# Kernel tuning notes

Measured on AMD Instinct MI355X. Metric: run time of the kernel, lower is better.

The kernel has to match this reference:

```python
import jax, jax.numpy as jnp
import numpy as np

B, S, D, H = 4, 2048, 1024, 16
DH = D // H
MAX_SEQ = 2048
OUT = 1024


def setup_inputs() -> dict:
    key = jax.random.key(0)
    ks = jax.random.split(key, 10)
    inp = {
        "x": jax.random.normal(ks[0], (B, S, D), dtype=jnp.float32),
        "src_key_padding_mask": jnp.ones((B, S), dtype=jnp.float32),  # 1 = valid token
        "pos_emb": jax.random.normal(ks[1], (1, MAX_SEQ, D), dtype=jnp.float32),
        "ln_gamma": jnp.ones((D,), dtype=jnp.float32),
        "ln_beta": jnp.zeros((D,), dtype=jnp.float32),
        "in_proj_weight": jax.random.normal(ks[2], (3 * D, D), dtype=jnp.float32) * (1.0 / np.sqrt(D)),
        "in_proj_bias": jnp.zeros((3 * D,), dtype=jnp.float32),
        "out_proj_weight": jax.random.normal(ks[3], (D, D), dtype=jnp.float32) * (1.0 / np.sqrt(D)),
        "out_proj_bias": jnp.zeros((D,), dtype=jnp.float32),
        "to_out_weight": jax.random.normal(ks[4], (OUT, D), dtype=jnp.float32) * (1.0 / np.sqrt(D)),
        "to_out_bias": jnp.zeros((OUT,), dtype=jnp.float32),
    }
    return inp


def _layernorm(x, gamma, beta, eps=1e-5):
    mu = jnp.mean(x, axis=-1, keepdims=True)
    var = jnp.mean(jnp.square(x - mu), axis=-1, keepdims=True)
    return (x - mu) * jax.lax.rsqrt(var + eps) * gamma + beta


def reference(x, src_key_padding_mask, pos_emb, ln_gamma, ln_beta,
              in_proj_weight, in_proj_bias, out_proj_weight, out_proj_bias,
              to_out_weight, to_out_bias):
    seq = x.shape[1]
    xn = _layernorm(x, ln_gamma, ln_beta)
    xp = xn + pos_emb[:, :seq, :]  # [B,S,D]

    # PyTorch quirk: 1.0 - mask.long() is a FLOAT tensor -> treated as ADDITIVE mask.
    add_mask = (1.0 - src_key_padding_mask)[:, None, None, :]  # [B,1,1,S]

    qkv = xp @ in_proj_weight.T + in_proj_bias  # [B,S,3D]
    q, k, v = jnp.split(qkv, 3, axis=-1)
    # [B,H,S,DH]
    q = q.reshape(B, seq, H, DH).transpose(0, 2, 1, 3)
    k = k.reshape(B, seq, H, DH).transpose(0, 2, 1, 3)
    v = v.reshape(B, seq, H, DH).transpose(0, 2, 1, 3)

    scores = jnp.einsum("bhqd,bhkd->bhqk", q, k) / jnp.sqrt(jnp.float32(DH))
    scores = scores + add_mask
    attn = jax.nn.softmax(scores, axis=-1)
    o = jnp.einsum("bhqk,bhkd->bhqd", attn, v)  # [B,H,S,DH]
    o = o.transpose(0, 2, 1, 3).reshape(B, seq, D)
    attn_out = o @ out_proj_weight.T + out_proj_bias

    return (xp + attn_out) @ to_out_weight.T + to_out_bias
```

## Files before the change

kernel.cpp:

```cpp
#include <hip/hip_runtime.h>
#include <stdint.h>
#include <stddef.h>

typedef unsigned short u16;
typedef __bf16 bf16x8 __attribute__((ext_vector_type(8)));
typedef float floatx4 __attribute__((ext_vector_type(4)));

#define B_  4
#define S_  2048
#define D_  1024
#define H_  16
#define DH_ 64

__device__ __forceinline__ float b2f(u16 u) {
  union { unsigned u; float f; } c; c.u = ((unsigned)u) << 16; return c.f;
}
__device__ __forceinline__ u16 f2b(float f) {
  union { float f; unsigned u; } c; c.f = f;
  unsigned u = c.u;
  u += 0x7fffu + ((u >> 16) & 1u);
  return (u16)(u >> 16);
}

__device__ __forceinline__ void gld_lds16(const u16* g, u16* l) {
  __builtin_amdgcn_global_load_lds(
      (const __attribute__((address_space(1))) unsigned int*)g,
      (__attribute__((address_space(3))) unsigned int*)l, 16, 0, 0);
}

__device__ __forceinline__ unsigned cvtpk(float lo, float hi) {
  unsigned r;
  asm("v_cvt_pk_bf16_f32 %0, %1, %2" : "=v"(r) : "v"(lo), "v"(hi));
  return r;
}

#define PL32(a, b) asm("v_permlane32_swap_b32 %0, %1" : "+v"(a), "+v"(b))
#define PL16(a, b) asm("v_permlane16_swap_b32 %0, %1" : "+v"(a), "+v"(b))

union B8 { unsigned u[4]; bf16x8 v; };

__global__ __launch_bounds__(256) void cvt_f32_bf16(
    const float* __restrict__ src, u16* __restrict__ dst, int n)
{
  int i = (blockIdx.x * 256 + threadIdx.x) * 4;
  if (i >= n) return;
  float4 v = *(const float4*)(src + i);
  u16 o[4] __attribute__((aligned(8)));
  o[0] = f2b(v.x); o[1] = f2b(v.y); o[2] = f2b(v.z); o[3] = f2b(v.w);
  *(uint2*)(dst + i) = *(uint2*)o;
}

__global__ __launch_bounds__(256) void ln_pos_kernel(
    const float* __restrict__ x, const float* __restrict__ pos,
    const float* __restrict__ gamma, const float* __restrict__ beta,
    u16* __restrict__ xp)
{
  const int row = blockIdx.x;
  const int s = row & (S_ - 1);
  const int t = threadIdx.x;
  const int lane = t & 63, w = t >> 6;

  float4 xv = *(const float4*)(x + (size_t)row * D_ + t * 4);
  float f[4] = {xv.x, xv.y, xv.z, xv.w};
  float sum = f[0] + f[1] + f[2] + f[3];
  float sq  = f[0]*f[0] + f[1]*f[1] + f[2]*f[2] + f[3]*f[3];
#pragma unroll
  for (int m = 1; m < 64; m <<= 1) {
    sum += __shfl_xor(sum, m);
    sq  += __shfl_xor(sq, m);
  }
  __shared__ float red[8];
  if (lane == 0) { red[w] = sum; red[4 + w] = sq; }
  __syncthreads();
  sum = red[0] + red[1] + red[2] + red[3];
  sq  = red[4] + red[5] + red[6] + red[7];
  const float mu = sum * (1.f / D_);
  const float rstd = rsqrtf(fmaxf(sq * (1.f / D_) - mu * mu, 0.f) + 1e-5f);

  float4 gv = *(const float4*)(gamma + t * 4);
  float4 bv = *(const float4*)(beta + t * 4);
  float4 pv = *(const float4*)(pos + (size_t)s * D_ + t * 4);
  float g[4] = {gv.x, gv.y, gv.z, gv.w};
  float bb[4] = {bv.x, bv.y, bv.z, bv.w};
  float pp[4] = {pv.x, pv.y, pv.z, pv.w};
  u16 ov[4] __attribute__((aligned(8)));
#pragma unroll
  for (int i = 0; i < 4; ++i)
    ov[i] = f2b((f[i] - mu) * rstd * g[i] + bb[i] + pp[i]);
  *(uint2*)(xp + (size_t)row * D_ + t * 4) = *(uint2*)ov;
}

template<int HAS_BIAS, int HAS_RES, int OUT_F32>
__global__ __launch_bounds__(256) void gemm_bt(
    const u16* A, const u16* __restrict__ Bm,
    const float* __restrict__ bias, const u16* res,
    void* Cv, int M, int N, int K, int lda, int ldc)
{
  __shared__ u16 As[2][128 * 32];
  __shared__ u16 Bs[2][128 * 32];
  const int tid = threadIdx.x;
  const int lane = tid & 63, w = tid >> 6;
  const int quad = lane >> 4, l4 = lane & 15;
  const int wm = (w >> 1) * 64, wn = (w & 1) * 64;
  const int m0 = blockIdx.y * 128, n0 = blockIdx.x * 128;

  const u16* Ag = A + (size_t)m0 * lda;
  const u16* Bg = Bm + (size_t)n0 * K;

  const int s0 = tid, s1 = tid + 256;
  const int r0 = s0 >> 2, c0 = ((s0 & 3) - (r0 >> 1)) & 3;
  const int r1 = s1 >> 2, c1 = ((s1 & 3) - (r1 >> 1)) & 3;
  const int pA = (quad + (l4 >> 1)) & 3;

  floatx4 acc[4][4] = {};

  const int nk = K >> 5;
  gld_lds16(Ag + (size_t)r0 * lda + c0 * 8, &As[0][s0 * 8]);
  gld_lds16(Ag + (size_t)r1 * lda + c1 * 8, &As[0][s1 * 8]);
  gld_lds16(Bg + (size_t)r0 * K + c0 * 8, &Bs[0][s0 * 8]);
  gld_lds16(Bg + (size_t)r1 * K + c1 * 8, &Bs[0][s1 * 8]);
  __syncthreads();

  for (int kk = 0; kk < nk; ++kk) {
    const int cur = kk & 1;
    if (kk + 1 < nk) {
      const int k0 = (kk + 1) << 5;
      gld_lds16(Ag + (size_t)r0 * lda + k0 + c0 * 8, &As[cur ^ 1][s0 * 8]);
      gld_lds16(Ag + (size_t)r1 * lda + k0 + c1 * 8, &As[cur ^ 1][s1 * 8]);
      gld_lds16(Bg + (size_t)r0 * K + k0 + c0 * 8, &Bs[cur ^ 1][s0 * 8]);
      gld_lds16(Bg + (size_t)r1 * K + k0 + c1 * 8, &Bs[cur ^ 1][s1 * 8]);
    }
    bf16x8 af[4], bfr[4];
#pragma unroll
    for (int i = 0; i < 4; ++i)
      af[i] = *(const bf16x8*)&As[cur][(wm + i * 16 + l4) * 32 + pA * 8];
#pragma unroll
    for (int j = 0; j < 4; ++j)
      bfr[j] = *(const bf16x8*)&Bs[cur][(wn + j * 16 + l4) * 32 + pA * 8];
#pragma unroll
    for (int i = 0; i < 4; ++i)
#pragma unroll
      for (int j = 0; j < 4; ++j)
        acc[i][j] = __builtin_amdgcn_mfma_f32_16x16x32_bf16(af[i], bfr[j], acc[i][j], 0, 0, 0);
    __syncthreads();
  }

#pragma unroll
  for (int i = 0; i < 4; ++i) {
#pragma unroll
    for (int j = 0; j < 4; ++j) {
      const int col = n0 + wn + j * 16 + l4;
      float bvv = 0.f;
      if (HAS_BIAS) bvv = bias[col];
#pragma unroll
      for (int r = 0; r < 4; ++r) {
        const int row = m0 + wm + i * 16 + quad * 4 + r;
        float v = acc[i][j][r] + bvv;
        if (HAS_RES) v += b2f(res[(size_t)row * ldc + col]);
        v = fminf(fmaxf(v, -60000.f), 60000.f);
        if (OUT_F32) ((float*)Cv)[(size_t)row * ldc + col] = v;
        else         ((u16*)Cv)[(size_t)row * ldc + col] = f2b(v);
      }
    }
  }
}

__global__ __launch_bounds__(256, 3) void attn_kernel(
    u16* qkv, const float* __restrict__ mask)
{
  __shared__ u16 Ks[2][64 * 64];
  __shared__ u16 Vt[2][64 * 72];

  const int tid = threadIdx.x;
  const int lane = tid & 63, w = tid >> 6;
  const int quad = lane >> 4, l4 = lane & 15;
  const int qb = blockIdx.x;
  const int bh = blockIdx.y;
  const int b = bh >> 4, h = bh & 15;
  const int q0 = qb * 128;

  const size_t rstr = 3 * D_;
  u16* qbase = qkv + (size_t)b * S_ * rstr + h * DH_;

  bf16x8 qfrag[2][2];
#pragma unroll
  for (int qi = 0; qi < 2; ++qi) {
    const u16* qp = qbase + (size_t)(q0 + w * 32 + qi * 16 + l4) * rstr + quad * 8;
    qfrag[qi][0] = *(const bf16x8*)(qp);
    qfrag[qi][1] = *(const bf16x8*)(qp + 32);
  }

  const u16* kbase0 = qkv + (size_t)b * S_ * rstr + D_ + h * DH_;
  const u16* vbase0 = kbase0 + D_;
  const int vs = tid & 63, vd0 = (tid >> 6) * 16;

  floatx4 acc_o[2][4] = {};
  float l_run[2] = {0.f, 0.f};
  u16 vreg[16] __attribute__((aligned(16)));

  {
#pragma unroll
    for (int t = 0; t < 2; ++t) {
      int sidx = tid + t * 256;
      int rr = sidx >> 3, ch = ((sidx & 7) - rr) & 7;
      gld_lds16(kbase0 + (size_t)rr * rstr + ch * 8, &Ks[0][sidx * 8]);
    }
    const u16* vp = vbase0 + (size_t)vs * rstr + vd0;
    *(uint4*)(vreg)     = *(const uint4*)(vp);
    *(uint4*)(vreg + 8) = *(const uint4*)(vp + 8);
  }
  __syncthreads();
#pragma unroll
  for (int d = 0; d < 16; ++d) Vt[0][(vd0 + d) * 72 + vs] = vreg[d];
  __syncthreads();

  int cur = 0;
  for (int j = 0; j < 32; ++j) {
    if (j < 31) {
      const u16* vp = vbase0 + ((size_t)(j + 1) * 64 + vs) * rstr + vd0;
      *(uint4*)(vreg)     = *(const uint4*)(vp);
      *(uint4*)(vreg + 8) = *(const uint4*)(vp + 8);
      const u16* kb = kbase0 + (size_t)(j + 1) * 64 * rstr;
#pragma unroll
      for (int t = 0; t < 2; ++t) {
        int sidx = tid + t * 256;
        int rr = sidx >> 3, ch = ((sidx & 7) - rr) & 7;
        gld_lds16(kb + (size_t)rr * rstr + ch * 8, &Ks[cur ^ 1][sidx * 8]);
      }
    }

    floatx4 accs[2][4] = {};
#pragma unroll
    for (int kc = 0; kc < 2; ++kc)
#pragma unroll
      for (int tj = 0; tj < 4; ++tj) {
        const int rk = tj * 16 + l4;
        bf16x8 kf = *(const bf16x8*)&Ks[cur][rk * 64 + (((kc * 4 + quad) + rk) & 7) * 8];
        accs[0][tj] = __builtin_amdgcn_mfma_f32_16x16x32_bf16(kf, qfrag[0][kc], accs[0][tj], 0, 0, 0);
        accs[1][tj] = __builtin_amdgcn_mfma_f32_16x16x32_bf16(kf, qfrag[1][kc], accs[1][tj], 0, 0, 0);
      }

    const float* mrow = mask + (size_t)b * S_ + j * 64 + quad * 4;
    float4 mv[4];
#pragma unroll
    for (int tj = 0; tj < 4; ++tj) mv[tj] = *(const float4*)(mrow + tj * 16);
    unsigned pk[2][4][2];
#pragma unroll
    for (int qi = 0; qi < 2; ++qi) {
      float rsum = 0.f;
#pragma unroll
      for (int tj = 0; tj < 4; ++tj) {
        float p0 = __expf(fminf(fmaf(accs[qi][tj][0], 0.125f, 1.0f - mv[tj].x), 30.f));
        float p1 = __expf(fminf(fmaf(accs[qi][tj][1], 0.125f, 1.0f - mv[tj].y), 30.f));
        float p2 = __expf(fminf(fmaf(accs[qi][tj][2], 0.125f, 1.0f - mv[tj].z), 30.f));
        float p3 = __expf(fminf(fmaf(accs[qi][tj][3], 0.125f, 1.0f - mv[tj].w), 30.f));
        rsum += (p0 + p1) + (p2 + p3);
        pk[qi][tj][0] = cvtpk(p0, p1);
        pk[qi][tj][1] = cvtpk(p2, p3);
      }
      rsum += __shfl_xor(rsum, 16);
      rsum += __shfl_xor(rsum, 32);
      l_run[qi] += rsum;
    }

#pragma unroll
    for (int kc = 0; kc < 2; ++kc) {
      bf16x8 bfr[4];
#pragma unroll
      for (int tn = 0; tn < 4; ++tn)
        bfr[tn] = *(const bf16x8*)&Vt[cur][(tn * 16 + l4) * 72 + kc * 32 + quad * 8];
#pragma unroll
      for (int qi = 0; qi < 2; ++qi) {
        unsigned x0 = pk[qi][2 * kc][0], x1 = pk[qi][2 * kc + 1][0];
        unsigned y0 = pk[qi][2 * kc][1], y1 = pk[qi][2 * kc + 1][1];
        PL32(x0, x1); PL32(y0, y1);
        PL16(x0, x1); PL16(y0, y1);
        B8 pa; pa.u[0] = x0; pa.u[1] = y0; pa.u[2] = x1; pa.u[3] = y1;
        __builtin_amdgcn_s_setprio(1);
#pragma unroll
        for (int tn = 0; tn < 4; ++tn)
          acc_o[qi][tn] = __builtin_amdgcn_mfma_f32_16x16x32_bf16(pa.v, bfr[tn], acc_o[qi][tn], 0, 0, 0);
        __builtin_amdgcn_s_setprio(0);
      }
    }

    if (j < 31) {
#pragma unroll
      for (int d = 0; d < 16; ++d) Vt[cur ^ 1][(vd0 + d) * 72 + vs] = vreg[d];
    }

    __syncthreads();
    cur ^= 1;
  }

#pragma unroll
  for (int qi = 0; qi < 2; ++qi) {
    float inv[4];
#pragma unroll
    for (int r = 0; r < 4; ++r) inv[r] = 1.0f / __shfl(l_run[qi], quad * 4 + r);
#pragma unroll
    for (int tn = 0; tn < 4; ++tn) {
#pragma unroll
      for (int r = 0; r < 4; ++r) {
        const int row = q0 + w * 32 + qi * 16 + quad * 4 + r;
        const int col = h * DH_ + tn * 16 + l4;
        qkv[((size_t)b * S_ + row) * rstr + col] = f2b(acc_o[qi][tn][r] * inv[r]);
      }
    }
  }
}

extern "C" void kernel_launch(void* const* d_in, const int* in_sizes, int n_in,
                              void* d_out, int out_size, void* d_ws, size_t ws_size,
                              hipStream_t stream) {
  const float* x    = (const float*)d_in[0];
  const float* mask = (const float*)d_in[1];
  const float* pos  = (const float*)d_in[2];
  const float* gam  = (const float*)d_in[3];
  const float* bet  = (const float*)d_in[4];
  const float* wqkv = (const float*)d_in[5];
  const float* bqkv = (const float*)d_in[6];
  const float* wo   = (const float*)d_in[7];
  const float* bo   = (const float*)d_in[8];
  const float* wt   = (const float*)d_in[9];
  const float* bt   = (const float*)d_in[10];
  float* out = (float*)d_out;

  char* ws = (char*)d_ws;
  u16* qkvb = (u16*)(ws);
  u16* xp   = (u16*)(ws + (size_t)50331648);

  u16* wqkv_b = (u16*)d_out;
  u16* wo_b   = (u16*)((char*)d_out + (size_t)6291456);
  u16* wt_b   = qkvb;

  const int nqkv = 3 * D_ * D_;
  const int nd   = D_ * D_;

  cvt_f32_bf16<<<nqkv / 1024, 256, 0, stream>>>(wqkv, wqkv_b, nqkv);
  cvt_f32_bf16<<<nd   / 1024, 256, 0, stream>>>(wo,   wo_b,   nd);
  ln_pos_kernel<<<B_ * S_, 256, 0, stream>>>(x, pos, gam, bet, xp);
  gemm_bt<1, 0, 0><<<dim3(3 * D_ / 128, B_ * S_ / 128), 256, 0, stream>>>(
      xp, wqkv_b, bqkv, nullptr, qkvb, B_ * S_, 3 * D_, D_, D_, 3 * D_);
  attn_kernel<<<dim3(S_ / 128, B_ * H_), 256, 0, stream>>>(qkvb, mask);
  gemm_bt<1, 1, 0><<<dim3(D_ / 128, B_ * S_ / 128), 256, 0, stream>>>(
      qkvb, wo_b, bo, xp, xp, B_ * S_, D_, D_, 3 * D_, D_);
  cvt_f32_bf16<<<nd / 1024, 256, 0, stream>>>(wt, wt_b, nd);
  gemm_bt<1, 0, 1><<<dim3(D_ / 128, B_ * S_ / 128), 256, 0, stream>>>(
      xp, wt_b, bt, nullptr, out, B_ * S_, D_, D_, D_, D_);
}
```

Measured before the change: 396.9 us.

## Use exp2 softmax, MFMA row sums, and swizzled GEMM block order

The attention softmax now folds log2(e) into the score scale and the mask term and calls the raw v_exp_f32 instruction, replacing __expf. The row sums are no longer built with adds and cross-lane shuffles; an extra MFMA against a vector of bf16 ones accumulates them on the matrix unit. This also means the denominator is summed from the bf16-rounded probabilities, the same values used in P·V. Separately, the GEMM remaps block indices in groups of 8 to change L2 locality, adding integer divide and modulo work per block.

```diff
diff --git a/kernel.cpp b/kernel.cpp
--- a/kernel.cpp
+++ b/kernel.cpp
@@ -32,6 +32,10 @@
   unsigned r;
   asm("v_cvt_pk_bf16_f32 %0, %1, %2" : "=v"(r) : "v"(lo), "v"(hi));
   return r;
+}
+
+__device__ __forceinline__ float fexp2(float x) {
+  float r; asm("v_exp_f32 %0, %1" : "=v"(r) : "v"(x)); return r;
 }
 
 #define PL32(a, b) asm("v_permlane32_swap_b32 %0, %1" : "+v"(a), "+v"(b))
@@ -102,7 +106,11 @@
   const int lane = tid & 63, w = tid >> 6;
   const int quad = lane >> 4, l4 = lane & 15;
   const int wm = (w >> 1) * 64, wn = (w & 1) * 64;
-  const int m0 = blockIdx.y * 128, n0 = blockIdx.x * 128;
+
+  const int gx = gridDim.x;
+  int lin = blockIdx.y * gx + blockIdx.x;
+  lin = (lin & 7) * ((gx * gridDim.y) >> 3) + (lin >> 3);
+  const int m0 = (lin / gx) * 128, n0 = (lin % gx) * 128;
 
   const u16* Ag = A + (size_t)m0 * lda;
   const u16* Bg = Bm + (size_t)n0 * K;
@@ -194,8 +202,11 @@
   const u16* vbase0 = kbase0 + D_;
   const int vs = tid & 63, vd0 = (tid >> 6) * 16;
 
+  B8 ones;
+  ones.u[0] = ones.u[1] = ones.u[2] = ones.u[3] = 0x3f803f80u;
+
   floatx4 acc_o[2][4] = {};
-  float l_run[2] = {0.f, 0.f};
+  floatx4 acc_l[2] = {};
   u16 vreg[16] __attribute__((aligned(16)));
 
   {
@@ -241,26 +252,27 @@
       }
 
     const float* mrow = mask + (size_t)b * S_ + j * 64 + quad * 4;
-    float4 mv[4];
-#pragma unroll
-    for (int tj = 0; tj < 4; ++tj) mv[tj] = *(const float4*)(mrow + tj * 16);
+    float mterm[4][4];
+#pragma unroll
+    for (int tj = 0; tj < 4; ++tj) {
+      float4 mv = *(const float4*)(mrow + tj * 16);
+      mterm[tj][0] = fmaf(mv.x, -1.44269504f, 1.44269504f);
+      mterm[tj][1] = fmaf(mv.y, -1.44269504f, 1.44269504f);
+      mterm[tj][2] = fmaf(mv.z, -1.44269504f, 1.44269504f);
+      mterm[tj][3] = fmaf(mv.w, -1.44269504f, 1.44269504f);
+    }
     unsigned pk[2][4][2];
 #pragma unroll
     for (int qi = 0; qi < 2; ++qi) {
-      float rsum = 0.f;
 #pragma unroll
       for (int tj = 0; tj < 4; ++tj) {
-        float p0 = __expf(fminf(fmaf(accs[qi][tj][0], 0.125f, 1.0f - mv[tj].x), 30.f));
-        float p1 = __expf(fminf(fmaf(accs[qi][tj][1], 0.125f, 1.0f - mv[tj].y), 30.f));
-        float p2 = __expf(fminf(fmaf(accs[qi][tj][2], 0.125f, 1.0f - mv[tj].z), 30.f));
-        float p3 = __expf(fminf(fmaf(accs[qi][tj][3], 0.125f, 1.0f - mv[tj].w), 30.f));
-        rsum += (p0 + p1) + (p2 + p3);
+        float p0 = fexp2(fminf(fmaf(accs[qi][tj][0], 0.18033688f, mterm[tj][0]), 43.3f));
+        float p1 = fexp2(fminf(fmaf(accs[qi][tj][1], 0.18033688f, mterm[tj][1]), 43.3f));
+        float p2 = fexp2(fminf(fmaf(accs[qi][tj][2], 0.18033688f, mterm[tj][2]), 43.3f));
+        float p3 = fexp2(fminf(fmaf(accs[qi][tj][3], 0.18033688f, mterm[tj][3]), 43.3f));
         pk[qi][tj][0] = cvtpk(p0, p1);
         pk[qi][tj][1] = cvtpk(p2, p3);
       }
-      rsum += __shfl_xor(rsum, 16);
-      rsum += __shfl_xor(rsum, 32);
-      l_run[qi] += rsum;
     }
 
 #pragma unroll
@@ -280,6 +292,7 @@
 #pragma unroll
         for (int tn = 0; tn < 4; ++tn)
           acc_o[qi][tn] = __builtin_amdgcn_mfma_f32_16x16x32_bf16(pa.v, bfr[tn], acc_o[qi][tn], 0, 0, 0);
+        acc_l[qi] = __builtin_amdgcn_mfma_f32_16x16x32_bf16(pa.v, ones.v, acc_l[qi], 0, 0, 0);
         __builtin_amdgcn_s_setprio(0);
       }
     }
@@ -297,7 +310,7 @@
   for (int qi = 0; qi < 2; ++qi) {
     float inv[4];
 #pragma unroll
-    for (int r = 0; r < 4; ++r) inv[r] = 1.0f / __shfl(l_run[qi], quad * 4 + r);
+    for (int r = 0; r < 4; ++r) inv[r] = 1.0f / acc_l[qi][r];
 #pragma unroll
     for (int tn = 0; tn < 4; ++tn) {
 #pragma unroll
```

After: 384.0 us, median of 2. 3.3% less time.
